# Kernel tuning notes

Measured on AMD Instinct MI355X. Metric: run time of the kernel, lower is better.

## Reference

```python
import jax, jax.numpy as jnp
import numpy as np

MARGIN = 1.0
NUM_CLASSES = 28
K = 16


def setup_inputs() -> dict:
    key = jax.random.key(0)
    k1, k2, k3 = jax.random.split(key, 3)
    B, C, D = 256, 28, 2048
    # multilabel prediction probabilities
    inp = jax.random.uniform(k1, (B, C), dtype=jnp.float32)
    # sparse multilabel targets (p~0.02 so minority-class selection via
    # cumsum(counts) <= 0.5*num_classes is non-degenerate)
    target = jax.random.bernoulli(k2, 0.02, (B, C)).astype(jnp.int32)
    # embeddings used for the mined triplets
    X = jax.random.normal(k3, (B, D), dtype=jnp.float32)
    return {"input": inp, "target": target, "X": X}


def _crl_loss(inp, X, target):
    B = inp.shape[0]
    y = target.astype(inp.dtype)

    # --- get_minority_classes ---
    counts = y.sum(0)                                   # [C] per-class positive counts
    order = jnp.argsort(counts)                         # ascending by count
    cum = jnp.cumsum(counts[order])
    keep_sorted = cum <= 0.5 * NUM_CLASSES              # threshold as in source
    rank = jnp.argsort(order)                           # position of class c in sorted order
    minority = keep_sorted[rank] & (counts > 1)         # [C] bool mask over classes

    # pairwise L1 distances between embeddings: Dm[i,j] = sum_d |X_i - X_j|
    Dm = jnp.abs(X[:, None, :] - X[None, :, :]).sum(-1)  # [B,B]

    pos_mask = target == 1                              # [B,C]
    inf = jnp.inf
    pos_key = jnp.where(pos_mask, inp, inf)             # [B,C] sort keys for positives
    neg_key = jnp.where(pos_mask, -inf, inp)            # [B,C] sort keys for negatives

    def per_class(pk, nk, pm, m_c):
        # hardest negatives of this class: largest predicted prob (neg_idxs[-k:])
        nvals, nidx = jax.lax.top_k(nk, K)              # [K]
        nvalid = jnp.isfinite(nvals).astype(Dm.dtype)
        n_n = nvalid.sum()                              # min(k, n_neg)
        dn_anchor = (Dm[:, nidx] * nvalid).sum(-1)      # [B] sum_j |X_i - X_negj|_1

        def per_anchor(i):
            keys = pk.at[i].set(inf)                    # mask[idx] = 0: exclude anchor
            # hardest positives: smallest predicted prob (sorted[:k])
            pvals, pidx = jax.lax.top_k(-keys, K)
            pvalid = jnp.isfinite(pvals).astype(Dm.dtype)
            n_p = pvalid.sum()                          # min(k, n_pos - 1)
            dp = (Dm[i, pidx] * pvalid).sum()
            w = (pm[i] & m_c).astype(Dm.dtype)          # anchor is a positive of a minority class
            # each positive appears in n_n triplets, each negative in n_p triplets
            return w * n_n * dp, w * n_p * dn_anchor[i]

        dps, dns = jax.vmap(per_anchor)(jnp.arange(B))
        return dps.sum(), dns.sum()

    dp_c, dn_c = jax.vmap(per_class, in_axes=(1, 1, 1, 0))(pos_key, neg_key, pos_mask, minority)
    # TripletLoss with F.l1_loss(size_average=False) sums over all triplet elements,
    # so distance_positive / distance_negative are scalars -> scalar relu loss.
    return jax.nn.relu(dp_c.sum() - dn_c.sum() + MARGIN)


def reference(input, target, X):
    return _crl_loss(input, X, target)
```

## Files before the change

### kernel.cpp

```cpp
#include <hip/hip_runtime.h>
#include <math.h>

typedef unsigned int u32;
typedef unsigned long long u64;

#define BB 256
#define CC 28
#define DD 2048
#define KK 16
#define GA 14

struct Sync {
  float acc[2];
  u32 ticket;
  u32 pad;
};

__global__ __launch_bounds__(256) void k_main(const float* __restrict__ inp,
                                              const int* __restrict__ target,
                                              const float* __restrict__ X,
                                              Sync* __restrict__ S,
                                              float* __restrict__ out) {
  const int c = blockIdx.x;
  const int a = blockIdx.y;
  const int tid = threadIdx.x;
  const int wave = tid >> 6, lane = tid & 63;

  __shared__ u32 s_bits[BB];
  __shared__ u32 s_pb[BB];
  __shared__ int s_cw[4][CC];
  __shared__ int s_counts[CC];
  __shared__ int s_act[CC];
  __shared__ int s_pw[4];
  __shared__ int s_S[16], s_N[16], s_anchor;
  __shared__ float s_red[8];

  u32 pb = 0;
  const int4* t4 = (const int4*)(target + tid * CC);
#pragma unroll
  for (int k = 0; k < 7; ++k) {
    int4 w = t4[k];
    pb |= (u32)(w.x != 0) << (4 * k) | (u32)(w.y != 0) << (4 * k + 1) |
          (u32)(w.z != 0) << (4 * k + 2) | (u32)(w.w != 0) << (4 * k + 3);
  }
  s_pb[tid] = pb;
  const u32 b = __float_as_uint(inp[tid * CC + c]);
  s_bits[tid] = b;

#pragma unroll
  for (int c2 = 0; c2 < CC; ++c2) {
    u64 bl = __ballot((pb >> c2) & 1u);
    if (lane == 0) s_cw[wave][c2] = __popcll(bl);
  }
  const int p = (pb >> c) & 1;
  const u64 bp = __ballot(p != 0);
  if (lane == 0) s_pw[wave] = __popcll(bp);
  __syncthreads();
  if (tid < CC)
    s_counts[tid] = s_cw[0][tid] + s_cw[1][tid] + s_cw[2][tid] + s_cw[3][tid];
  __syncthreads();

  if (tid < CC) {
    const int mt = s_counts[tid];
    int cum = 0;
#pragma unroll
    for (int c2 = 0; c2 < CC; ++c2) {
      const int m2 = s_counts[c2];
      cum += (m2 < mt || (m2 == mt && c2 <= tid)) ? m2 : 0;
    }
    s_act[tid] = ((2 * cum <= CC) && (mt > 1)) ? mt : 0;
  }
  __syncthreads();

  const int m = s_counts[c];
  const bool active = (s_act[c] > 0) && (a < m);
  int total = 0;
  if (tid == 0) {
#pragma unroll
    for (int c2 = 0; c2 < CC; ++c2) total += s_act[c2];
  }

  if (!active) {
    if (c == 0 && a == 0 && tid == 0 && total == 0)
      out[0] = 1.0f;
    return;
  }

  int rank = 0;
  for (int j = 0; j < BB; ++j) {
    const u32 bj = s_bits[j];
    const int pj = (s_pb[j] >> c) & 1;
    const bool bpos = (bj < b) || (bj == b && j < tid);
    const bool bneg = (bj > b) || (bj == b && j < tid);
    rank += p ? ((pj && bpos) ? 1 : 0) : ((!pj && bneg) ? 1 : 0);
  }
  if (p) {
    if (rank < 16) s_S[rank] = tid;
    int idx = __popcll(bp & ((1ull << lane) - 1ull));
#pragma unroll
    for (int w2 = 0; w2 < 4; ++w2)
      if (w2 < wave) idx += s_pw[w2];
    if (idx == a) s_anchor = tid;
  } else {
    if (rank < KK) s_N[rank] = tid;
  }
  __syncthreads();

  const int anchor = s_anchor;
  const int NP = m - 1;
  const int NN = min(KK, BB - m);
  int idx_a = 0;
  for (int u = 0; u < m; ++u)
    if (s_S[u] == anchor) idx_a = u;

  const float4* Xa = (const float4*)(X + (size_t)anchor * DD);
  float4 A[8];
#pragma unroll
  for (int q = 0; q < 8; ++q) A[q] = Xa[q * 64 + lane];

  float dp = 0.f, dn = 0.f;
  for (int pidx = wave; pidx < NP + NN; pidx += 4) {
    const bool isdp = pidx < NP;
    const int j = isdp ? s_S[pidx + (pidx >= idx_a ? 1 : 0)] : s_N[pidx - NP];
    const float4* Xj = (const float4*)(X + (size_t)j * DD);
    float partial = 0.f;
#pragma unroll
    for (int q = 0; q < 8; ++q) {
      const float4 b4 = Xj[q * 64 + lane];
      partial += fabsf(A[q].x - b4.x) + fabsf(A[q].y - b4.y) +
                 fabsf(A[q].z - b4.z) + fabsf(A[q].w - b4.w);
    }
#pragma unroll
    for (int s = 1; s < 64; s <<= 1) partial += __shfl_xor(partial, s);
    if (isdp) dp += partial; else dn += partial;
  }
  if (lane == 0) { s_red[2 * wave] = dp; s_red[2 * wave + 1] = dn; }
  __syncthreads();

  if (tid == 0) {
    const float dpT = s_red[0] + s_red[2] + s_red[4] + s_red[6];
    const float dnT = s_red[1] + s_red[3] + s_red[5] + s_red[7];
    atomicAdd(&S->acc[0], (float)NN * dpT);
    atomicAdd(&S->acc[1], (float)NP * dnT);
    __threadfence();
    const u32 tk = atomicAdd(&S->ticket, 1u);
    if (tk == (u32)(total - 1)) {
      __threadfence();
      const float a0 = atomicAdd(&S->acc[0], 0.f);
      const float a1 = atomicAdd(&S->acc[1], 0.f);
      out[0] = fmaxf(a0 - a1 + 1.0f, 0.0f);
    }
  }
}

extern "C" void kernel_launch(void* const* d_in, const int* in_sizes, int n_in,
                              void* d_out, int out_size, void* d_ws, size_t ws_size,
                              hipStream_t stream) {
  (void)in_sizes; (void)n_in; (void)out_size; (void)ws_size;
  const float* inp    = (const float*)d_in[0];
  const int*   target = (const int*)d_in[1];
  const float* X      = (const float*)d_in[2];
  float* out = (float*)d_out;
  Sync* S = (Sync*)d_ws;

  hipMemsetAsync(S, 0, sizeof(Sync), stream);
  k_main<<<dim3(CC, GA), 256, 0, stream>>>(inp, target, X, S, out);
}
```

Before: 82.75 us.

## Replace atomic ticket reduction and memset with per-block partials plus final kernel

After: 81.17 us. No clear change (-1.9%).

```diff
diff --git a/kernel.cpp b/kernel.cpp
--- a/kernel.cpp
+++ b/kernel.cpp
@@ -10,17 +10,10 @@
 #define KK 16
 #define GA 14
 
-struct Sync {
-  float acc[2];
-  u32 ticket;
-  u32 pad;
-};
-
-__global__ __launch_bounds__(256) void k_main(const float* __restrict__ inp,
-                                              const int* __restrict__ target,
-                                              const float* __restrict__ X,
-                                              Sync* __restrict__ S,
-                                              float* __restrict__ out) {
+__global__ __launch_bounds__(256) void k_all(const float* __restrict__ inp,
+                                             const int* __restrict__ target,
+                                             const float* __restrict__ X,
+                                             float* __restrict__ part) {
   const int c = blockIdx.x;
   const int a = blockIdx.y;
   const int tid = threadIdx.x;
@@ -30,9 +23,8 @@
   __shared__ u32 s_pb[BB];
   __shared__ int s_cw[4][CC];
   __shared__ int s_counts[CC];
-  __shared__ int s_act[CC];
+  __shared__ int s_S[16], s_N[16], s_anchor;
   __shared__ int s_pw[4];
-  __shared__ int s_S[16], s_N[16], s_anchor;
   __shared__ float s_red[8];
 
   u32 pb = 0;
@@ -60,29 +52,20 @@
     s_counts[tid] = s_cw[0][tid] + s_cw[1][tid] + s_cw[2][tid] + s_cw[3][tid];
   __syncthreads();
 
-  if (tid < CC) {
-    const int mt = s_counts[tid];
-    int cum = 0;
+  const int m = s_counts[c];
+  int cum = 0;
 #pragma unroll
-    for (int c2 = 0; c2 < CC; ++c2) {
-      const int m2 = s_counts[c2];
-      cum += (m2 < mt || (m2 == mt && c2 <= tid)) ? m2 : 0;
-    }
-    s_act[tid] = ((2 * cum <= CC) && (mt > 1)) ? mt : 0;
+  for (int c2 = 0; c2 < CC; ++c2) {
+    const int m2 = s_counts[c2];
+    cum += (m2 < m || (m2 == m && c2 <= c)) ? m2 : 0;
   }
-  __syncthreads();
-
-  const int m = s_counts[c];
-  const bool active = (s_act[c] > 0) && (a < m);
-  int total = 0;
-  if (tid == 0) {
-#pragma unroll
-    for (int c2 = 0; c2 < CC; ++c2) total += s_act[c2];
-  }
+  const bool active = (2 * cum <= CC) && (m > 1) && (a < m);
 
   if (!active) {
-    if (c == 0 && a == 0 && tid == 0 && total == 0)
-      out[0] = 1.0f;
+    if (tid == 0) {
+      part[2 * (c * GA + a)] = 0.f;
+      part[2 * (c * GA + a) + 1] = 0.f;
+    }
     return;
   }
 
@@ -138,18 +121,33 @@
   __syncthreads();
 
   if (tid == 0) {
+    part[2 * (c * GA + a)]     = (float)NN * (s_red[0] + s_red[2] + s_red[4] + s_red[6]);
+    part[2 * (c * GA + a) + 1] = (float)NP * (s_red[1] + s_red[3] + s_red[5] + s_red[7]);
+  }
+}
+
+__global__ __launch_bounds__(256) void k_final(const float* __restrict__ part,
+                                               float* __restrict__ out) {
+  const int tid = threadIdx.x;
+  const int wave = tid >> 6, lane = tid & 63;
+  __shared__ float s_red[8];
+
+  float dp = 0.f, dn = 0.f;
+  for (int t = tid; t < CC * GA; t += 256) {
+    dp += part[2 * t];
+    dn += part[2 * t + 1];
+  }
+#pragma unroll
+  for (int s = 1; s < 64; s <<= 1) {
+    dp += __shfl_xor(dp, s);
+    dn += __shfl_xor(dn, s);
+  }
+  if (lane == 0) { s_red[2 * wave] = dp; s_red[2 * wave + 1] = dn; }
+  __syncthreads();
+  if (tid == 0) {
     const float dpT = s_red[0] + s_red[2] + s_red[4] + s_red[6];
     const float dnT = s_red[1] + s_red[3] + s_red[5] + s_red[7];
-    atomicAdd(&S->acc[0], (float)NN * dpT);
-    atomicAdd(&S->acc[1], (float)NP * dnT);
-    __threadfence();
-    const u32 tk = atomicAdd(&S->ticket, 1u);
-    if (tk == (u32)(total - 1)) {
-      __threadfence();
-      const float a0 = atomicAdd(&S->acc[0], 0.f);
-      const float a1 = atomicAdd(&S->acc[1], 0.f);
-      out[0] = fmaxf(a0 - a1 + 1.0f, 0.0f);
-    }
+    out[0] = fmaxf(dpT - dnT + 1.0f, 0.0f);
   }
 }
 
@@ -161,8 +159,8 @@
   const int*   target = (const int*)d_in[1];
   const float* X      = (const float*)d_in[2];
   float* out = (float*)d_out;
-  Sync* S = (Sync*)d_ws;
+  float* part = (float*)d_ws;
 
-  hipMemsetAsync(S, 0, sizeof(Sync), stream);
-  k_main<<<dim3(CC, GA), 256, 0, stream>>>(inp, target, X, S, out);
+  k_all<<<dim3(CC, GA), 256, 0, stream>>>(inp, target, X, part);
+  k_final<<<1, 256, 0, stream>>>(part, out);
 }
```
